# Kernel tuning notes

Hardware: AMD Instinct MI355X
Metric: run time of the kernel (lower is better)

## Reference

```python
import jax, jax.numpy as jnp
import numpy as np

NUM_PHONEMES = 512
D = 128  # embed_dim == hidden_channels == out_channels (forced by residuals)
N = 50000
E = 500000
PAD_ID = 0
LN_EPS = 1e-5


def setup_inputs() -> dict:
    key = jax.random.key(0)
    ks = jax.random.split(key, 12)
    node_ids = jax.random.randint(ks[0], (N,), 0, NUM_PHONEMES)
    edge_index = jax.random.randint(ks[1], (2, E), 0, N)
    emb = jax.random.normal(ks[2], (NUM_PHONEMES, D), jnp.float32) * 0.05
    emb = emb.at[PAD_ID].set(0.0)  # padding_idx row zeroed
    W1 = jax.random.normal(ks[3], (D, D), jnp.float32) * (1.0 / np.sqrt(D))
    b1 = jnp.zeros((D,), jnp.float32)
    W2 = jax.random.normal(ks[4], (D, D), jnp.float32) * (1.0 / np.sqrt(D))
    b2 = jnp.zeros((D,), jnp.float32)
    g1 = jnp.ones((D,), jnp.float32)
    beta1 = jnp.zeros((D,), jnp.float32)
    g2 = jnp.ones((D,), jnp.float32)
    beta2 = jnp.zeros((D,), jnp.float32)
    return {"node_ids": node_ids, "edge_index": edge_index, "emb": emb,
            "W1": W1, "b1": b1, "W2": W2, "b2": b2,
            "g1": g1, "beta1": beta1, "g2": g2, "beta2": beta2}


def _gcn_conv(x, src, dst, W, b):
    """PyG GCNConv with add_self_loops=True, normalize=True.
    out = D^{-1/2} (A + I) D^{-1/2} (x W) + b, deg computed after self-loops."""
    n = x.shape[0]
    loop = jnp.arange(n, dtype=src.dtype)
    src_f = jnp.concatenate([src, loop])  # [E+N]
    dst_f = jnp.concatenate([dst, loop])
    deg = jax.ops.segment_sum(jnp.ones_like(dst_f, dtype=x.dtype), dst_f,
                              num_segments=n)  # >=1 due to self-loops
    dis = jax.lax.rsqrt(deg)
    norm = dis[src_f] * dis[dst_f]  # [E+N]
    h = x @ W  # [N, D_out]
    msg = h[src_f] * norm[:, None]  # [E+N, D_out] gather (memory-bound)
    out = jax.ops.segment_sum(msg, dst_f, num_segments=n)  # scatter-add
    return out + b


def _layernorm(x, g, b):
    mu = jnp.mean(x, axis=-1, keepdims=True)
    var = jnp.mean(jnp.square(x - mu), axis=-1, keepdims=True)
    return (x - mu) * jax.lax.rsqrt(var + LN_EPS) * g + b


def reference(node_ids, edge_index, emb, W1, b1, W2, b2, g1, beta1, g2, beta2):
    src, dst = edge_index[0], edge_index[1]
    x = emb[node_ids]  # embedding lookup [N, D]
    h1 = _gcn_conv(x, src, dst, W1, b1)
    x = _layernorm(x + h1, g1, beta1)  # dropout is identity in eval mode
    h2 = _gcn_conv(x, src, dst, W2, b2)
    x = _layernorm(x + h2, g2, beta2)
    return x
```

## Files before the change

kernel.cpp:

```cpp
#include <hip/hip_runtime.h>

#define DD 128
#define CAP 32
#define SPILL_MAX 4096

typedef __attribute__((ext_vector_type(8))) short short8;
typedef __attribute__((ext_vector_type(4))) float float4v;

static __device__ __forceinline__ unsigned short f2bf(float x) {
    unsigned u = __builtin_bit_cast(unsigned, x);
    u += 0x7fffu + ((u >> 16) & 1u);
    return (unsigned short)(u >> 16);
}
static __device__ __forceinline__ float bflo(unsigned u) {
    return __builtin_bit_cast(float, u << 16);
}
static __device__ __forceinline__ float bfhi(unsigned u) {
    return __builtin_bit_cast(float, u & 0xffff0000u);
}

__global__ __launch_bounds__(256) void k_init(const float* __restrict__ emb,
                                              const float* __restrict__ W1,
                                              const float* __restrict__ W2,
                                              unsigned* __restrict__ embW1b,
                                              unsigned short* __restrict__ Wb,
                                              int* __restrict__ zero_dst, int NZ) {
    int blk = blockIdx.x;
    if (blk < 128) {
        int w = threadIdx.x >> 6;
        int t = threadIdx.x & 63;
        int p = blk * 4 + w;
        int c0 = t * 2, c1 = t * 2 + 1;
        float s0 = 0.f, s1 = 0.f;
#pragma unroll 8
        for (int k = 0; k < DD; k++) {
            float e = emb[p * DD + k];
            s0 += e * W1[k * DD + c0];
            s1 += e * W1[k * DD + c1];
        }
        embW1b[p * 64 + t] = (unsigned)f2bf(s0) | ((unsigned)f2bf(s1) << 16);
    } else if (blk < 136) {
        int t = (blk - 128) * 256 + threadIdx.x;
        int nt = t >> 8, ks = (t >> 6) & 3, lane = t & 63;
        int n = nt * 16 + (lane & 15);
        int kbase = ks * 32 + (lane >> 4) * 8;
        unsigned short* o = Wb + (size_t)t * 8;
#pragma unroll
        for (int j = 0; j < 8; j++)
            o[j] = f2bf(W2[(kbase + j) * DD + n]);
    } else {
        int base = (blk - 136) * 1024 + threadIdx.x * 4;
        if (base + 3 < NZ) {
            *(int4*)(zero_dst + base) = make_int4(0, 0, 0, 0);
        } else {
            if (base + 0 < NZ) zero_dst[base + 0] = 0;
            if (base + 1 < NZ) zero_dst[base + 1] = 0;
            if (base + 2 < NZ) zero_dst[base + 2] = 0;
        }
    }
}

__global__ void k_bucket(const int* __restrict__ src, const int* __restrict__ dst,
                         const int* __restrict__ node_ids,
                         int* __restrict__ cursor, unsigned* __restrict__ recs,
                         int* __restrict__ spillCnt, int* __restrict__ spill_d,
                         int* __restrict__ spill_r, int E) {
    int base = (blockIdx.x * blockDim.x + threadIdx.x) * 4;
    if (base >= E) return;
#pragma unroll
    for (int u = 0; u < 4; u++) {
        int e = base + u;
        if (e >= E) break;
        int s = src[e], d = dst[e];
        unsigned rec = (unsigned)s | ((unsigned)node_ids[s] << 16);
        int pos = atomicAdd(&cursor[d], 1);
        if (pos < CAP) {
            recs[(size_t)d * CAP + pos] = rec;
        } else {
            int sp = atomicAdd(spillCnt, 1);
            if (sp < SPILL_MAX) { spill_d[sp] = d; spill_r[sp] = (int)rec; }
        }
    }
}

__global__ __launch_bounds__(256) void k_node1g(const int* __restrict__ cursor,
                                                const unsigned* __restrict__ recs,
                                                const int* __restrict__ node_ids,
                                                const float* __restrict__ emb,
                                                const unsigned* __restrict__ embW1b,
                                                const int* __restrict__ spillCnt,
                                                const int* __restrict__ spill_d,
                                                const int* __restrict__ spill_r,
                                                const float* __restrict__ b1,
                                                const float* __restrict__ g1,
                                                const float* __restrict__ beta1,
                                                const unsigned short* __restrict__ Wb,
                                                unsigned* __restrict__ x1b,
                                                unsigned short* __restrict__ hb, int N) {
    __shared__ unsigned tile[16 * 68];
    int wv = threadIdx.x >> 6;
    int lane = threadIdx.x & 63;
    int qtr = lane >> 4;
    int l = lane & 15;
    int qbase = lane & 48;
    int base16 = blockIdx.x * 16;
    int i = base16 + wv * 4 + qtr;
    if (i < N) {
        int dg = cursor[i];
        int r0 = i * CAP;
        int r1 = r0 + ((dg < CAP) ? dg : CAP);
        int c = l * 8;
        float a0 = 0.f, a1 = 0.f, a2 = 0.f, a3 = 0.f, a4 = 0.f, a5 = 0.f, a6 = 0.f, a7 = 0.f;
        for (int j0 = r0; j0 < r1; j0 += 16) {
            int pidx = j0 + l;
            unsigned rv = recs[(pidx < r1) ? pidx : (r1 - 1)];
            int lim = r1 - j0;
#pragma unroll
            for (int q = 0; q < 16; q++) {
                unsigned rec = __shfl(rv, qbase + q, 64);
                int s = rec & 0xFFFFu;
                float n = rsqrtf((float)cursor[s] + 1.0f);
                n = (q < lim) ? n : 0.f;
                uint4 a = *(const uint4*)(embW1b + ((rec >> 16) & 511u) * 64 + l * 4);
                a0 += bflo(a.x) * n; a1 += bfhi(a.x) * n;
                a2 += bflo(a.y) * n; a3 += bfhi(a.y) * n;
                a4 += bflo(a.z) * n; a5 += bfhi(a.z) * n;
                a6 += bflo(a.w) * n; a7 += bfhi(a.w) * n;
            }
        }
        if (dg > CAP) {
            int sc = *spillCnt; if (sc > SPILL_MAX) sc = SPILL_MAX;
            for (int j = 0; j < sc; j++) {
                if (spill_d[j] == i) {
                    unsigned rec = (unsigned)spill_r[j];
                    int s = rec & 0xFFFFu;
                    float n = rsqrtf((float)cursor[s] + 1.0f);
                    uint4 a = *(const uint4*)(embW1b + ((rec >> 16) & 511u) * 64 + l * 4);
                    a0 += bflo(a.x) * n; a1 += bfhi(a.x) * n;
                    a2 += bflo(a.y) * n; a3 += bfhi(a.y) * n;
                    a4 += bflo(a.z) * n; a5 += bfhi(a.z) * n;
                    a6 += bflo(a.w) * n; a7 += bfhi(a.w) * n;
                }
            }
        }
        float di = rsqrtf((float)dg + 1.0f);
        int pid = node_ids[i];
        float4 ev0 = *(const float4*)(emb + (size_t)pid * DD + c);
        float4 ev1 = *(const float4*)(emb + (size_t)pid * DD + c + 4);
        uint4 hw = *(const uint4*)(embW1b + pid * 64 + l * 4);
        float4 bb0 = *(const float4*)(b1 + c);
        float4 bb1 = *(const float4*)(b1 + c + 4);
        float v0 = ev0.x + di * (a0 + di * bflo(hw.x)) + bb0.x;
        float v1 = ev0.y + di * (a1 + di * bfhi(hw.x)) + bb0.y;
        float v2 = ev0.z + di * (a2 + di * bflo(hw.y)) + bb0.z;
        float v3 = ev0.w + di * (a3 + di * bfhi(hw.y)) + bb0.w;
        float v4 = ev1.x + di * (a4 + di * bflo(hw.z)) + bb1.x;
        float v5 = ev1.y + di * (a5 + di * bfhi(hw.z)) + bb1.y;
        float v6 = ev1.z + di * (a6 + di * bflo(hw.w)) + bb1.z;
        float v7 = ev1.w + di * (a7 + di * bfhi(hw.w)) + bb1.w;
        float sum = v0 + v1 + v2 + v3 + v4 + v5 + v6 + v7;
#pragma unroll
        for (int o = 8; o >= 1; o >>= 1) sum += __shfl_xor(sum, o, 64);
        float mu = sum * (1.f / DD);
        float d0 = v0 - mu, d1 = v1 - mu, d2 = v2 - mu, d3 = v3 - mu;
        float d4 = v4 - mu, d5 = v5 - mu, d6 = v6 - mu, d7 = v7 - mu;
        float ss = d0 * d0 + d1 * d1 + d2 * d2 + d3 * d3 + d4 * d4 + d5 * d5 + d6 * d6 + d7 * d7;
#pragma unroll
        for (int o = 8; o >= 1; o >>= 1) ss += __shfl_xor(ss, o, 64);
        float r = rsqrtf(ss * (1.f / DD) + 1e-5f);
        float4 gg0 = *(const float4*)(g1 + c);
        float4 gg1 = *(const float4*)(g1 + c + 4);
        float4 be0 = *(const float4*)(beta1 + c);
        float4 be1 = *(const float4*)(beta1 + c + 4);
        float o0 = d0 * r * gg0.x + be0.x;
        float o1 = d1 * r * gg0.y + be0.y;
        float o2 = d2 * r * gg0.z + be0.z;
        float o3 = d3 * r * gg0.w + be0.w;
        float o4 = d4 * r * gg1.x + be1.x;
        float o5 = d5 * r * gg1.y + be1.y;
        float o6 = d6 * r * gg1.z + be1.z;
        float o7 = d7 * r * gg1.w + be1.w;
        uint4 pk;
        pk.x = (unsigned)f2bf(o0) | ((unsigned)f2bf(o1) << 16);
        pk.y = (unsigned)f2bf(o2) | ((unsigned)f2bf(o3) << 16);
        pk.z = (unsigned)f2bf(o4) | ((unsigned)f2bf(o5) << 16);
        pk.w = (unsigned)f2bf(o6) | ((unsigned)f2bf(o7) << 16);
        *(uint4*)(x1b + (size_t)i * 64 + l * 4) = pk;
        *(uint4*)(tile + (wv * 4 + qtr) * 68 + l * 4) = pk;
    }
    __syncthreads();
    int m = l;
    int quad = qtr;
    short8 afr[4];
    const char* tb = (const char*)tile;
#pragma unroll
    for (int ks = 0; ks < 4; ks++)
        afr[ks] = *(const short8*)(tb + m * 272 + ks * 64 + quad * 16);
    float dr[4];
    {
        int rb = base16 + quad * 4;
        const int4 cv = *(const int4*)(cursor + rb);
        dr[0] = rsqrtf((float)cv.x + 1.f);
        dr[1] = rsqrtf((float)cv.y + 1.f);
        dr[2] = rsqrtf((float)cv.z + 1.f);
        dr[3] = rsqrtf((float)cv.w + 1.f);
    }
    const short8* bp = (const short8*)Wb;
#pragma unroll
    for (int t = 0; t < 2; t++) {
        int nt = wv * 2 + t;
        float4v acc = {0.f, 0.f, 0.f, 0.f};
#pragma unroll
        for (int ks = 0; ks < 4; ks++) {
            short8 bfr = bp[(nt * 4 + ks) * 64 + lane];
            acc = __builtin_amdgcn_mfma_f32_16x16x32_bf16(afr[ks], bfr, acc, 0, 0, 0);
        }
        int col = nt * 16 + m;
#pragma unroll
        for (int r = 0; r < 4; r++) {
            int row = base16 + quad * 4 + r;
            if (row < N) hb[(size_t)row * DD + col] = f2bf(acc[r] * dr[r]);
        }
    }
}

__global__ __launch_bounds__(256) void k_node2(const int* __restrict__ cursor,
                                               const unsigned* __restrict__ recs,
                                               const unsigned* __restrict__ x1b,
                                               const unsigned* __restrict__ h2b,
                                               const int* __restrict__ spillCnt,
                                               const int* __restrict__ spill_d,
                                               const int* __restrict__ spill_r,
                                               const float* __restrict__ b2,
                                               const float* __restrict__ g2,
                                               const float* __restrict__ beta2,
                                               float* __restrict__ out, int N) {
    int gid = blockIdx.x * blockDim.x + threadIdx.x;
    int wave = gid >> 6;
    int lane = threadIdx.x & 63;
    int qtr = lane >> 4;
    int l = lane & 15;
    int qbase = lane & 48;
    int i = wave * 4 + qtr;
    if (i >= N) return;
    int dg = cursor[i];
    int r0 = i * CAP;
    int r1 = r0 + ((dg < CAP) ? dg : CAP);
    int c = l * 8;
    float a0 = 0.f, a1 = 0.f, a2 = 0.f, a3 = 0.f, a4 = 0.f, a5 = 0.f, a6 = 0.f, a7 = 0.f;
    for (int j0 = r0; j0 < r1; j0 += 16) {
        int pidx = j0 + l;
        unsigned rv = recs[(pidx < r1) ? pidx : (r1 - 1)];
        int lim = r1 - j0;
#pragma unroll
        for (int q = 0; q < 16; q++) {
            unsigned s = __shfl(rv, qbase + q, 64) & 0xFFFFu;
            float w = (q < lim) ? 1.f : 0.f;
            uint4 a = *(const uint4*)(h2b + (size_t)s * 64 + l * 4);
            a0 += bflo(a.x) * w; a1 += bfhi(a.x) * w;
            a2 += bflo(a.y) * w; a3 += bfhi(a.y) * w;
            a4 += bflo(a.z) * w; a5 += bfhi(a.z) * w;
            a6 += bflo(a.w) * w; a7 += bfhi(a.w) * w;
        }
    }
    if (dg > CAP) {
        int sc = *spillCnt; if (sc > SPILL_MAX) sc = SPILL_MAX;
        for (int j = 0; j < sc; j++) {
            if (spill_d[j] == i) {
                unsigned s = (unsigned)spill_r[j] & 0xFFFFu;
                uint4 a = *(const uint4*)(h2b + (size_t)s * 64 + l * 4);
                a0 += bflo(a.x); a1 += bfhi(a.x);
                a2 += bflo(a.y); a3 += bfhi(a.y);
                a4 += bflo(a.z); a5 += bfhi(a.z);
                a6 += bflo(a.w); a7 += bfhi(a.w);
            }
        }
    }
    float di = rsqrtf((float)dg + 1.0f);
    uint4 xv = *(const uint4*)(x1b + (size_t)i * 64 + l * 4);
    uint4 hv = *(const uint4*)(h2b + (size_t)i * 64 + l * 4);
    float4 bb0 = *(const float4*)(b2 + c);
    float4 bb1 = *(const float4*)(b2 + c + 4);
    float v0 = bflo(xv.x) + di * (a0 + bflo(hv.x)) + bb0.x;
    float v1 = bfhi(xv.x) + di * (a1 + bfhi(hv.x)) + bb0.y;
    float v2 = bflo(xv.y) + di * (a2 + bflo(hv.y)) + bb0.z;
    float v3 = bfhi(xv.y) + di * (a3 + bfhi(hv.y)) + bb0.w;
    float v4 = bflo(xv.z) + di * (a4 + bflo(hv.z)) + bb1.x;
    float v5 = bfhi(xv.z) + di * (a5 + bfhi(hv.z)) + bb1.y;
    float v6 = bflo(xv.w) + di * (a6 + bflo(hv.w)) + bb1.z;
    float v7 = bfhi(xv.w) + di * (a7 + bfhi(hv.w)) + bb1.w;
    float sum = v0 + v1 + v2 + v3 + v4 + v5 + v6 + v7;
#pragma unroll
    for (int o = 8; o >= 1; o >>= 1) sum += __shfl_xor(sum, o, 64);
    float mu = sum * (1.f / DD);
    float d0 = v0 - mu, d1 = v1 - mu, d2 = v2 - mu, d3 = v3 - mu;
    float d4 = v4 - mu, d5 = v5 - mu, d6 = v6 - mu, d7 = v7 - mu;
    float ss = d0 * d0 + d1 * d1 + d2 * d2 + d3 * d3 + d4 * d4 + d5 * d5 + d6 * d6 + d7 * d7;
#pragma unroll
    for (int o = 8; o >= 1; o >>= 1) ss += __shfl_xor(ss, o, 64);
    float r = rsqrtf(ss * (1.f / DD) + 1e-5f);
    float4 gg0 = *(const float4*)(g2 + c);
    float4 gg1 = *(const float4*)(g2 + c + 4);
    float4 be0 = *(const float4*)(beta2 + c);
    float4 be1 = *(const float4*)(beta2 + c + 4);
    float4 o0, o1;
    o0.x = d0 * r * gg0.x + be0.x;
    o0.y = d1 * r * gg0.y + be0.y;
    o0.z = d2 * r * gg0.z + be0.z;
    o0.w = d3 * r * gg0.w + be0.w;
    o1.x = d4 * r * gg1.x + be1.x;
    o1.y = d5 * r * gg1.y + be1.y;
    o1.z = d6 * r * gg1.z + be1.z;
    o1.w = d7 * r * gg1.w + be1.w;
    *(float4*)(out + (size_t)i * DD + c) = o0;
    *(float4*)(out + (size_t)i * DD + c + 4) = o1;
}

extern "C" void kernel_launch(void* const* d_in, const int* in_sizes, int n_in,
                              void* d_out, int out_size, void* d_ws, size_t ws_size,
                              hipStream_t stream) {
    const int* node_ids = (const int*)d_in[0];
    const int* edge_index = (const int*)d_in[1];
    const float* emb   = (const float*)d_in[2];
    const float* W1    = (const float*)d_in[3];
    const float* b1    = (const float*)d_in[4];
    const float* W2    = (const float*)d_in[5];
    const float* b2    = (const float*)d_in[6];
    const float* g2    = (const float*)d_in[9];
    const float* g1    = (const float*)d_in[7];
    const float* beta1 = (const float*)d_in[8];
    const float* beta2 = (const float*)d_in[10];
    const int N = in_sizes[0];
    const int E = in_sizes[1] / 2;
    const int* srcp = edge_index;
    const int* dstp = edge_index + E;
    float* out = (float*)d_out;

    char* base = (char*)d_ws;
    size_t off = 0;
    auto carve = [&](size_t bytes) -> void* {
        void* p = base + off;
        off += (bytes + 255) & ~(size_t)255;
        return p;
    };
    int*      meta   = (int*)carve((size_t)(N + 17) * 4);
    int*      cursor = meta;
    int*      spillCnt = meta + N + 16;
    int*      spill_d = (int*)carve((size_t)SPILL_MAX * 4);
    int*      spill_r = (int*)carve((size_t)SPILL_MAX * 4);
    unsigned* recs   = (unsigned*)carve((size_t)N * CAP * 4);
    unsigned* embW1b = (unsigned*)carve((size_t)512 * 64 * 4);
    unsigned* x1b    = (unsigned*)carve((size_t)(N + 16) * 64 * 4);
    unsigned* h2b    = (unsigned*)carve((size_t)(N + 16) * 64 * 4);
    unsigned short* Wb = (unsigned short*)carve((size_t)DD * DD * 2);
    (void)ws_size; (void)n_in; (void)out_size;

    const int TB = 256;
    const int NZ = N + 17;
    const int Zb = (NZ + 1023) / 1024;

    k_init<<<136 + Zb, TB, 0, stream>>>(emb, W1, W2, embW1b, Wb, meta, NZ);
    k_bucket<<<(E + 1023) / 1024, TB, 0, stream>>>(srcp, dstp, node_ids, cursor, recs,
                                                   spillCnt, spill_d, spill_r, E);

    int blocks16 = (N + 15) / 16;
    k_node1g<<<blocks16, TB, 0, stream>>>(cursor, recs, node_ids, emb, embW1b,
                                          spillCnt, spill_d, spill_r,
                                          b1, g1, beta1, Wb, x1b, (unsigned short*)h2b, N);
    k_node2<<<blocks16, TB, 0, stream>>>(cursor, recs, x1b, h2b,
                                         spillCnt, spill_d, spill_r,
                                         b2, g2, beta2, out, N);
}
```

Baseline: 176.3 us.

## Aggregate-then-transform in layer two and fold edge bucketing into init kernel

Layer two now sums neighbor rows of x1 first, scaled by the symmetric norm, and then applies W2 with MFMA inside the same kernel that does the residual and LayerNorm. This removes the separate transformed-feature buffer h2b and its global write and read. Layer one becomes a plain gather+LayerNorm kernel with no MFMA. Edge bucketing moves into the init kernel as extra blocks, and the cursor zeroing becomes a hipMemsetAsync. The aggregated features are rounded to bf16 before the matmul, which adds a little rounding error.

```diff
diff --git a/kernel.cpp b/kernel.cpp
--- a/kernel.cpp
+++ b/kernel.cpp
@@ -24,7 +24,14 @@
                                               const float* __restrict__ W2,
                                               unsigned* __restrict__ embW1b,
                                               unsigned short* __restrict__ Wb,
-                                              int* __restrict__ zero_dst, int NZ) {
+                                              const int* __restrict__ src,
+                                              const int* __restrict__ dst,
+                                              const int* __restrict__ node_ids,
+                                              int* __restrict__ cursor,
+                                              unsigned* __restrict__ recs,
+                                              int* __restrict__ spillCnt,
+                                              int* __restrict__ spill_d,
+                                              int* __restrict__ spill_r, int E) {
     int blk = blockIdx.x;
     if (blk < 128) {
         int w = threadIdx.x >> 6;
@@ -49,192 +56,37 @@
         for (int j = 0; j < 8; j++)
             o[j] = f2bf(W2[(kbase + j) * DD + n]);
     } else {
-        int base = (blk - 136) * 1024 + threadIdx.x * 4;
-        if (base + 3 < NZ) {
-            *(int4*)(zero_dst + base) = make_int4(0, 0, 0, 0);
-        } else {
-            if (base + 0 < NZ) zero_dst[base + 0] = 0;
-            if (base + 1 < NZ) zero_dst[base + 1] = 0;
-            if (base + 2 < NZ) zero_dst[base + 2] = 0;
-        }
-    }
-}
-
-__global__ void k_bucket(const int* __restrict__ src, const int* __restrict__ dst,
-                         const int* __restrict__ node_ids,
-                         int* __restrict__ cursor, unsigned* __restrict__ recs,
-                         int* __restrict__ spillCnt, int* __restrict__ spill_d,
-                         int* __restrict__ spill_r, int E) {
-    int base = (blockIdx.x * blockDim.x + threadIdx.x) * 4;
-    if (base >= E) return;
-#pragma unroll
-    for (int u = 0; u < 4; u++) {
-        int e = base + u;
-        if (e >= E) break;
-        int s = src[e], d = dst[e];
-        unsigned rec = (unsigned)s | ((unsigned)node_ids[s] << 16);
-        int pos = atomicAdd(&cursor[d], 1);
-        if (pos < CAP) {
-            recs[(size_t)d * CAP + pos] = rec;
-        } else {
-            int sp = atomicAdd(spillCnt, 1);
-            if (sp < SPILL_MAX) { spill_d[sp] = d; spill_r[sp] = (int)rec; }
-        }
-    }
-}
-
-__global__ __launch_bounds__(256) void k_node1g(const int* __restrict__ cursor,
-                                                const unsigned* __restrict__ recs,
-                                                const int* __restrict__ node_ids,
-                                                const float* __restrict__ emb,
-                                                const unsigned* __restrict__ embW1b,
-                                                const int* __restrict__ spillCnt,
-                                                const int* __restrict__ spill_d,
-                                                const int* __restrict__ spill_r,
-                                                const float* __restrict__ b1,
-                                                const float* __restrict__ g1,
-                                                const float* __restrict__ beta1,
-                                                const unsigned short* __restrict__ Wb,
-                                                unsigned* __restrict__ x1b,
-                                                unsigned short* __restrict__ hb, int N) {
-    __shared__ unsigned tile[16 * 68];
-    int wv = threadIdx.x >> 6;
-    int lane = threadIdx.x & 63;
-    int qtr = lane >> 4;
-    int l = lane & 15;
-    int qbase = lane & 48;
-    int base16 = blockIdx.x * 16;
-    int i = base16 + wv * 4 + qtr;
-    if (i < N) {
-        int dg = cursor[i];
-        int r0 = i * CAP;
-        int r1 = r0 + ((dg < CAP) ? dg : CAP);
-        int c = l * 8;
-        float a0 = 0.f, a1 = 0.f, a2 = 0.f, a3 = 0.f, a4 = 0.f, a5 = 0.f, a6 = 0.f, a7 = 0.f;
-        for (int j0 = r0; j0 < r1; j0 += 16) {
-            int pidx = j0 + l;
-            unsigned rv = recs[(pidx < r1) ? pidx : (r1 - 1)];
-            int lim = r1 - j0;
-#pragma unroll
-            for (int q = 0; q < 16; q++) {
-                unsigned rec = __shfl(rv, qbase + q, 64);
-                int s = rec & 0xFFFFu;
-                float n = rsqrtf((float)cursor[s] + 1.0f);
-                n = (q < lim) ? n : 0.f;
-                uint4 a = *(const uint4*)(embW1b + ((rec >> 16) & 511u) * 64 + l * 4);
-                a0 += bflo(a.x) * n; a1 += bfhi(a.x) * n;
-                a2 += bflo(a.y) * n; a3 += bfhi(a.y) * n;
-                a4 += bflo(a.z) * n; a5 += bfhi(a.z) * n;
-                a6 += bflo(a.w) * n; a7 += bfhi(a.w) * n;
-            }
-        }
-        if (dg > CAP) {
-            int sc = *spillCnt; if (sc > SPILL_MAX) sc = SPILL_MAX;
-            for (int j = 0; j < sc; j++) {
-                if (spill_d[j] == i) {
-                    unsigned rec = (unsigned)spill_r[j];
-                    int s = rec & 0xFFFFu;
-                    float n = rsqrtf((float)cursor[s] + 1.0f);
-                    uint4 a = *(const uint4*)(embW1b + ((rec >> 16) & 511u) * 64 + l * 4);
-                    a0 += bflo(a.x) * n; a1 += bfhi(a.x) * n;
-                    a2 += bflo(a.y) * n; a3 += bfhi(a.y) * n;
-                    a4 += bflo(a.z) * n; a5 += bfhi(a.z) * n;
-                    a6 += bflo(a.w) * n; a7 += bfhi(a.w) * n;
-                }
-            }
-        }
-        float di = rsqrtf((float)dg + 1.0f);
-        int pid = node_ids[i];
-        float4 ev0 = *(const float4*)(emb + (size_t)pid * DD + c);
-        float4 ev1 = *(const float4*)(emb + (size_t)pid * DD + c + 4);
-        uint4 hw = *(const uint4*)(embW1b + pid * 64 + l * 4);
-        float4 bb0 = *(const float4*)(b1 + c);
-        float4 bb1 = *(const float4*)(b1 + c + 4);
-        float v0 = ev0.x + di * (a0 + di * bflo(hw.x)) + bb0.x;
-        float v1 = ev0.y + di * (a1 + di * bfhi(hw.x)) + bb0.y;
-        float v2 = ev0.z + di * (a2 + di * bflo(hw.y)) + bb0.z;
-        float v3 = ev0.w + di * (a3 + di * bfhi(hw.y)) + bb0.w;
-        float v4 = ev1.x + di * (a4 + di * bflo(hw.z)) + bb1.x;
-        float v5 = ev1.y + di * (a5 + di * bfhi(hw.z)) + bb1.y;
-        float v6 = ev1.z + di * (a6 + di * bflo(hw.w)) + bb1.z;
-        float v7 = ev1.w + di * (a7 + di * bfhi(hw.w)) + bb1.w;
-        float sum = v0 + v1 + v2 + v3 + v4 + v5 + v6 + v7;
-#pragma unroll
-        for (int o = 8; o >= 1; o >>= 1) sum += __shfl_xor(sum, o, 64);
-        float mu = sum * (1.f / DD);
-        float d0 = v0 - mu, d1 = v1 - mu, d2 = v2 - mu, d3 = v3 - mu;
-        float d4 = v4 - mu, d5 = v5 - mu, d6 = v6 - mu, d7 = v7 - mu;
-        float ss = d0 * d0 + d1 * d1 + d2 * d2 + d3 * d3 + d4 * d4 + d5 * d5 + d6 * d6 + d7 * d7;
-#pragma unroll
-        for (int o = 8; o >= 1; o >>= 1) ss += __shfl_xor(ss, o, 64);
-        float r = rsqrtf(ss * (1.f / DD) + 1e-5f);
-        float4 gg0 = *(const float4*)(g1 + c);
-        float4 gg1 = *(const float4*)(g1 + c + 4);
-        float4 be0 = *(const float4*)(beta1 + c);
-        float4 be1 = *(const float4*)(beta1 + c + 4);
-        float o0 = d0 * r * gg0.x + be0.x;
-        float o1 = d1 * r * gg0.y + be0.y;
-        float o2 = d2 * r * gg0.z + be0.z;
-        float o3 = d3 * r * gg0.w + be0.w;
-        float o4 = d4 * r * gg1.x + be1.x;
-        float o5 = d5 * r * gg1.y + be1.y;
-        float o6 = d6 * r * gg1.z + be1.z;
-        float o7 = d7 * r * gg1.w + be1.w;
-        uint4 pk;
-        pk.x = (unsigned)f2bf(o0) | ((unsigned)f2bf(o1) << 16);
-        pk.y = (unsigned)f2bf(o2) | ((unsigned)f2bf(o3) << 16);
-        pk.z = (unsigned)f2bf(o4) | ((unsigned)f2bf(o5) << 16);
-        pk.w = (unsigned)f2bf(o6) | ((unsigned)f2bf(o7) << 16);
-        *(uint4*)(x1b + (size_t)i * 64 + l * 4) = pk;
-        *(uint4*)(tile + (wv * 4 + qtr) * 68 + l * 4) = pk;
-    }
-    __syncthreads();
-    int m = l;
-    int quad = qtr;
-    short8 afr[4];
-    const char* tb = (const char*)tile;
-#pragma unroll
-    for (int ks = 0; ks < 4; ks++)
-        afr[ks] = *(const short8*)(tb + m * 272 + ks * 64 + quad * 16);
-    float dr[4];
-    {
-        int rb = base16 + quad * 4;
-        const int4 cv = *(const int4*)(cursor + rb);
-        dr[0] = rsqrtf((float)cv.x + 1.f);
-        dr[1] = rsqrtf((float)cv.y + 1.f);
-        dr[2] = rsqrtf((float)cv.z + 1.f);
-        dr[3] = rsqrtf((float)cv.w + 1.f);
-    }
-    const short8* bp = (const short8*)Wb;
-#pragma unroll
-    for (int t = 0; t < 2; t++) {
-        int nt = wv * 2 + t;
-        float4v acc = {0.f, 0.f, 0.f, 0.f};
-#pragma unroll
-        for (int ks = 0; ks < 4; ks++) {
-            short8 bfr = bp[(nt * 4 + ks) * 64 + lane];
-            acc = __builtin_amdgcn_mfma_f32_16x16x32_bf16(afr[ks], bfr, acc, 0, 0, 0);
-        }
-        int col = nt * 16 + m;
-#pragma unroll
-        for (int r = 0; r < 4; r++) {
-            int row = base16 + quad * 4 + r;
-            if (row < N) hb[(size_t)row * DD + col] = f2bf(acc[r] * dr[r]);
-        }
-    }
-}
-
-__global__ __launch_bounds__(256) void k_node2(const int* __restrict__ cursor,
+        int base = ((blk - 136) * 256 + threadIdx.x) * 4;
+        if (base >= E) return;
+#pragma unroll
+        for (int u = 0; u < 4; u++) {
+            int e = base + u;
+            if (e >= E) break;
+            int s = src[e], d = dst[e];
+            unsigned rec = (unsigned)s | ((unsigned)node_ids[s] << 16);
+            int pos = atomicAdd(&cursor[d], 1);
+            if (pos < CAP) {
+                recs[(size_t)d * CAP + pos] = rec;
+            } else {
+                int sp = atomicAdd(spillCnt, 1);
+                if (sp < SPILL_MAX) { spill_d[sp] = d; spill_r[sp] = (int)rec; }
+            }
+        }
+    }
+}
+
+__global__ __launch_bounds__(256) void k_node1(const int* __restrict__ cursor,
                                                const unsigned* __restrict__ recs,
-                                               const unsigned* __restrict__ x1b,
-                                               const unsigned* __restrict__ h2b,
+                                               const int* __restrict__ node_ids,
+                                               const float* __restrict__ emb,
+                                               const unsigned* __restrict__ embW1b,
                                                const int* __restrict__ spillCnt,
                                                const int* __restrict__ spill_d,
                                                const int* __restrict__ spill_r,
-                                               const float* __restrict__ b2,
-                                               const float* __restrict__ g2,
-                                               const float* __restrict__ beta2,
-                                               float* __restrict__ out, int N) {
+                                               const float* __restrict__ b1,
+                                               const float* __restrict__ g1,
+                                               const float* __restrict__ beta1,
+                                               unsigned* __restrict__ x1b, int N) {
     int gid = blockIdx.x * blockDim.x + threadIdx.x;
     int wave = gid >> 6;
     int lane = threadIdx.x & 63;
@@ -254,41 +106,203 @@
         int lim = r1 - j0;
 #pragma unroll
         for (int q = 0; q < 16; q++) {
-            unsigned s = __shfl(rv, qbase + q, 64) & 0xFFFFu;
-            float w = (q < lim) ? 1.f : 0.f;
-            uint4 a = *(const uint4*)(h2b + (size_t)s * 64 + l * 4);
-            a0 += bflo(a.x) * w; a1 += bfhi(a.x) * w;
-            a2 += bflo(a.y) * w; a3 += bfhi(a.y) * w;
-            a4 += bflo(a.z) * w; a5 += bfhi(a.z) * w;
-            a6 += bflo(a.w) * w; a7 += bfhi(a.w) * w;
+            unsigned rec = __shfl(rv, qbase + q, 64);
+            int s = rec & 0xFFFFu;
+            float n = rsqrtf((float)cursor[s] + 1.0f);
+            n = (q < lim) ? n : 0.f;
+            uint4 a = *(const uint4*)(embW1b + ((rec >> 16) & 511u) * 64 + l * 4);
+            a0 += bflo(a.x) * n; a1 += bfhi(a.x) * n;
+            a2 += bflo(a.y) * n; a3 += bfhi(a.y) * n;
+            a4 += bflo(a.z) * n; a5 += bfhi(a.z) * n;
+            a6 += bflo(a.w) * n; a7 += bfhi(a.w) * n;
         }
     }
     if (dg > CAP) {
         int sc = *spillCnt; if (sc > SPILL_MAX) sc = SPILL_MAX;
         for (int j = 0; j < sc; j++) {
             if (spill_d[j] == i) {
-                unsigned s = (unsigned)spill_r[j] & 0xFFFFu;
-                uint4 a = *(const uint4*)(h2b + (size_t)s * 64 + l * 4);
-                a0 += bflo(a.x); a1 += bfhi(a.x);
-                a2 += bflo(a.y); a3 += bfhi(a.y);
-                a4 += bflo(a.z); a5 += bfhi(a.z);
-                a6 += bflo(a.w); a7 += bfhi(a.w);
+                unsigned rec = (unsigned)spill_r[j];
+                int s = rec & 0xFFFFu;
+                float n = rsqrtf((float)cursor[s] + 1.0f);
+                uint4 a = *(const uint4*)(embW1b + ((rec >> 16) & 511u) * 64 + l * 4);
+                a0 += bflo(a.x) * n; a1 += bfhi(a.x) * n;
+                a2 += bflo(a.y) * n; a3 += bfhi(a.y) * n;
+                a4 += bflo(a.z) * n; a5 += bfhi(a.z) * n;
+                a6 += bflo(a.w) * n; a7 += bfhi(a.w) * n;
             }
         }
     }
     float di = rsqrtf((float)dg + 1.0f);
-    uint4 xv = *(const uint4*)(x1b + (size_t)i * 64 + l * 4);
-    uint4 hv = *(const uint4*)(h2b + (size_t)i * 64 + l * 4);
-    float4 bb0 = *(const float4*)(b2 + c);
-    float4 bb1 = *(const float4*)(b2 + c + 4);
-    float v0 = bflo(xv.x) + di * (a0 + bflo(hv.x)) + bb0.x;
-    float v1 = bfhi(xv.x) + di * (a1 + bfhi(hv.x)) + bb0.y;
-    float v2 = bflo(xv.y) + di * (a2 + bflo(hv.y)) + bb0.z;
-    float v3 = bfhi(xv.y) + di * (a3 + bfhi(hv.y)) + bb0.w;
-    float v4 = bflo(xv.z) + di * (a4 + bflo(hv.z)) + bb1.x;
-    float v5 = bfhi(xv.z) + di * (a5 + bfhi(hv.z)) + bb1.y;
-    float v6 = bflo(xv.w) + di * (a6 + bflo(hv.w)) + bb1.z;
-    float v7 = bfhi(xv.w) + di * (a7 + bfhi(hv.w)) + bb1.w;
+    int pid = node_ids[i];
+    float4 ev0 = *(const float4*)(emb + (size_t)pid * DD + c);
+    float4 ev1 = *(const float4*)(emb + (size_t)pid * DD + c + 4);
+    uint4 hw = *(const uint4*)(embW1b + pid * 64 + l * 4);
+    float4 bb0 = *(const float4*)(b1 + c);
+    float4 bb1 = *(const float4*)(b1 + c + 4);
+    float v0 = ev0.x + di * (a0 + di * bflo(hw.x)) + bb0.x;
+    float v1 = ev0.y + di * (a1 + di * bfhi(hw.x)) + bb0.y;
+    float v2 = ev0.z + di * (a2 + di * bflo(hw.y)) + bb0.z;
+    float v3 = ev0.w + di * (a3 + di * bfhi(hw.y)) + bb0.w;
+    float v4 = ev1.x + di * (a4 + di * bflo(hw.z)) + bb1.x;
+    float v5 = ev1.y + di * (a5 + di * bfhi(hw.z)) + bb1.y;
+    float v6 = ev1.z + di * (a6 + di * bflo(hw.w)) + bb1.z;
+    float v7 = ev1.w + di * (a7 + di * bfhi(hw.w)) + bb1.w;
+    float sum = v0 + v1 + v2 + v3 + v4 + v5 + v6 + v7;
+#pragma unroll
+    for (int o = 8; o >= 1; o >>= 1) sum += __shfl_xor(sum, o, 64);
+    float mu = sum * (1.f / DD);
+    float d0 = v0 - mu, d1 = v1 - mu, d2 = v2 - mu, d3 = v3 - mu;
+    float d4 = v4 - mu, d5 = v5 - mu, d6 = v6 - mu, d7 = v7 - mu;
+    float ss = d0 * d0 + d1 * d1 + d2 * d2 + d3 * d3 + d4 * d4 + d5 * d5 + d6 * d6 + d7 * d7;
+#pragma unroll
+    for (int o = 8; o >= 1; o >>= 1) ss += __shfl_xor(ss, o, 64);
+    float r = rsqrtf(ss * (1.f / DD) + 1e-5f);
+    float4 gg0 = *(const float4*)(g1 + c);
+    float4 gg1 = *(const float4*)(g1 + c + 4);
+    float4 be0 = *(const float4*)(beta1 + c);
+    float4 be1 = *(const float4*)(beta1 + c + 4);
+    float o0 = d0 * r * gg0.x + be0.x;
+    float o1 = d1 * r * gg0.y + be0.y;
+    float o2 = d2 * r * gg0.z + be0.z;
+    float o3 = d3 * r * gg0.w + be0.w;
+    float o4 = d4 * r * gg1.x + be1.x;
+    float o5 = d5 * r * gg1.y + be1.y;
+    float o6 = d6 * r * gg1.z + be1.z;
+    float o7 = d7 * r * gg1.w + be1.w;
+    uint4 pk;
+    pk.x = (unsigned)f2bf(o0) | ((unsigned)f2bf(o1) << 16);
+    pk.y = (unsigned)f2bf(o2) | ((unsigned)f2bf(o3) << 16);
+    pk.z = (unsigned)f2bf(o4) | ((unsigned)f2bf(o5) << 16);
+    pk.w = (unsigned)f2bf(o6) | ((unsigned)f2bf(o7) << 16);
+    *(uint4*)(x1b + (size_t)i * 64 + l * 4) = pk;
+}
+
+__global__ __launch_bounds__(256) void k_node2(const int* __restrict__ cursor,
+                                               const unsigned* __restrict__ recs,
+                                               const unsigned* __restrict__ x1b,
+                                               const int* __restrict__ spillCnt,
+                                               const int* __restrict__ spill_d,
+                                               const int* __restrict__ spill_r,
+                                               const float* __restrict__ b2,
+                                               const float* __restrict__ g2,
+                                               const float* __restrict__ beta2,
+                                               const unsigned short* __restrict__ Wb,
+                                               float* __restrict__ out, int N) {
+    __shared__ unsigned tileA[16 * 68];
+    __shared__ float tileH[16 * 132];
+    int wv = threadIdx.x >> 6;
+    int lane = threadIdx.x & 63;
+    int qtr = lane >> 4;
+    int l = lane & 15;
+    int qbase = lane & 48;
+    int base16 = blockIdx.x * 16;
+    int i = base16 + wv * 4 + qtr;
+    uint4 xv = make_uint4(0, 0, 0, 0);
+    float bb[8] = {0, 0, 0, 0, 0, 0, 0, 0};
+    int c = l * 8;
+    if (i < N) {
+        int dg = cursor[i];
+        int r0 = i * CAP;
+        int r1 = r0 + ((dg < CAP) ? dg : CAP);
+        float a0 = 0.f, a1 = 0.f, a2 = 0.f, a3 = 0.f, a4 = 0.f, a5 = 0.f, a6 = 0.f, a7 = 0.f;
+        for (int j0 = r0; j0 < r1; j0 += 16) {
+            int pidx = j0 + l;
+            unsigned rv = recs[(pidx < r1) ? pidx : (r1 - 1)];
+            int lim = r1 - j0;
+#pragma unroll
+            for (int q = 0; q < 16; q++) {
+                unsigned s = __shfl(rv, qbase + q, 64) & 0xFFFFu;
+                float n = rsqrtf((float)cursor[s] + 1.0f);
+                n = (q < lim) ? n : 0.f;
+                uint4 a = *(const uint4*)(x1b + (size_t)s * 64 + l * 4);
+                a0 += bflo(a.x) * n; a1 += bfhi(a.x) * n;
+                a2 += bflo(a.y) * n; a3 += bfhi(a.y) * n;
+                a4 += bflo(a.z) * n; a5 += bfhi(a.z) * n;
+                a6 += bflo(a.w) * n; a7 += bfhi(a.w) * n;
+            }
+        }
+        if (dg > CAP) {
+            int sc = *spillCnt; if (sc > SPILL_MAX) sc = SPILL_MAX;
+            for (int j = 0; j < sc; j++) {
+                if (spill_d[j] == i) {
+                    unsigned s = (unsigned)spill_r[j] & 0xFFFFu;
+                    float n = rsqrtf((float)cursor[s] + 1.0f);
+                    uint4 a = *(const uint4*)(x1b + (size_t)s * 64 + l * 4);
+                    a0 += bflo(a.x) * n; a1 += bfhi(a.x) * n;
+                    a2 += bflo(a.y) * n; a3 += bfhi(a.y) * n;
+                    a4 += bflo(a.z) * n; a5 += bfhi(a.z) * n;
+                    a6 += bflo(a.w) * n; a7 += bfhi(a.w) * n;
+                }
+            }
+        }
+        float di = rsqrtf((float)dg + 1.0f);
+        xv = *(const uint4*)(x1b + (size_t)i * 64 + l * 4);
+        float z0 = a0 + di * bflo(xv.x);
+        float z1 = a1 + di * bfhi(xv.x);
+        float z2 = a2 + di * bflo(xv.y);
+        float z3 = a3 + di * bfhi(xv.y);
+        float z4 = a4 + di * bflo(xv.z);
+        float z5 = a5 + di * bfhi(xv.z);
+        float z6 = a6 + di * bflo(xv.w);
+        float z7 = a7 + di * bfhi(xv.w);
+        uint4 pk;
+        pk.x = (unsigned)f2bf(z0) | ((unsigned)f2bf(z1) << 16);
+        pk.y = (unsigned)f2bf(z2) | ((unsigned)f2bf(z3) << 16);
+        pk.z = (unsigned)f2bf(z4) | ((unsigned)f2bf(z5) << 16);
+        pk.w = (unsigned)f2bf(z6) | ((unsigned)f2bf(z7) << 16);
+        *(uint4*)(tileA + (wv * 4 + qtr) * 68 + l * 4) = pk;
+        float4 t0 = *(const float4*)(b2 + c);
+        float4 t1 = *(const float4*)(b2 + c + 4);
+        bb[0] = t0.x; bb[1] = t0.y; bb[2] = t0.z; bb[3] = t0.w;
+        bb[4] = t1.x; bb[5] = t1.y; bb[6] = t1.z; bb[7] = t1.w;
+    }
+    __syncthreads();
+    {
+        int m = l;
+        int quad = qtr;
+        short8 afr[4];
+        const char* tb = (const char*)tileA;
+#pragma unroll
+        for (int ks = 0; ks < 4; ks++)
+            afr[ks] = *(const short8*)(tb + m * 272 + ks * 64 + quad * 16);
+        float dr[4];
+        {
+            int rb = base16 + quad * 4;
+            const int4 cv = *(const int4*)(cursor + rb);
+            dr[0] = rsqrtf((float)cv.x + 1.f);
+            dr[1] = rsqrtf((float)cv.y + 1.f);
+            dr[2] = rsqrtf((float)cv.z + 1.f);
+            dr[3] = rsqrtf((float)cv.w + 1.f);
+        }
+        const short8* bp = (const short8*)Wb;
+#pragma unroll
+        for (int t = 0; t < 2; t++) {
+            int nt = wv * 2 + t;
+            float4v acc = {0.f, 0.f, 0.f, 0.f};
+#pragma unroll
+            for (int ks = 0; ks < 4; ks++) {
+                short8 bfr = bp[(nt * 4 + ks) * 64 + lane];
+                acc = __builtin_amdgcn_mfma_f32_16x16x32_bf16(afr[ks], bfr, acc, 0, 0, 0);
+            }
+            int col = nt * 16 + m;
+#pragma unroll
+            for (int r = 0; r < 4; r++)
+                tileH[(quad * 4 + r) * 132 + col] = acc[r] * dr[r];
+        }
+    }
+    __syncthreads();
+    if (i >= N) return;
+    int row_local = wv * 4 + qtr;
+    float4 h0 = *(const float4*)(tileH + row_local * 132 + c);
+    float4 h1 = *(const float4*)(tileH + row_local * 132 + c + 4);
+    float v0 = bflo(xv.x) + h0.x + bb[0];
+    float v1 = bfhi(xv.x) + h0.y + bb[1];
+    float v2 = bflo(xv.y) + h0.z + bb[2];
+    float v3 = bfhi(xv.y) + h0.w + bb[3];
+    float v4 = bflo(xv.z) + h1.x + bb[4];
+    float v5 = bfhi(xv.z) + h1.y + bb[5];
+    float v6 = bflo(xv.w) + h1.z + bb[6];
+    float v7 = bfhi(xv.w) + h1.w + bb[7];
     float sum = v0 + v1 + v2 + v3 + v4 + v5 + v6 + v7;
 #pragma unroll
     for (int o = 8; o >= 1; o >>= 1) sum += __shfl_xor(sum, o, 64);
@@ -326,9 +340,9 @@
     const float* b1    = (const float*)d_in[4];
     const float* W2    = (const float*)d_in[5];
     const float* b2    = (const float*)d_in[6];
-    const float* g2    = (const float*)d_in[9];
     const float* g1    = (const float*)d_in[7];
     const float* beta1 = (const float*)d_in[8];
+    const float* g2    = (const float*)d_in[9];
     const float* beta2 = (const float*)d_in[10];
     const int N = in_sizes[0];
     const int E = in_sizes[1] / 2;
@@ -351,23 +365,24 @@
     unsigned* recs   = (unsigned*)carve((size_t)N * CAP * 4);
     unsigned* embW1b = (unsigned*)carve((size_t)512 * 64 * 4);
     unsigned* x1b    = (unsigned*)carve((size_t)(N + 16) * 64 * 4);
-    unsigned* h2b    = (unsigned*)carve((size_t)(N + 16) * 64 * 4);
     unsigned short* Wb = (unsigned short*)carve((size_t)DD * DD * 2);
     (void)ws_size; (void)n_in; (void)out_size;
 
     const int TB = 256;
-    const int NZ = N + 17;
-    const int Zb = (NZ + 1023) / 1024;
-
-    k_init<<<136 + Zb, TB, 0, stream>>>(emb, W1, W2, embW1b, Wb, meta, NZ);
-    k_bucket<<<(E + 1023) / 1024, TB, 0, stream>>>(srcp, dstp, node_ids, cursor, recs,
-                                                   spillCnt, spill_d, spill_r, E);
-
+    const int Hb = (E + 1023) / 1024;
+
+    hipMemsetAsync(meta, 0, (size_t)(N + 17) * 4, stream);
+    k_init<<<136 + Hb, TB, 0, stream>>>(emb, W1, W2, embW1b, Wb,
+                                        srcp, dstp, node_ids, cursor, recs,
+                                        spillCnt, spill_d, spill_r, E);
+
+    long long tn = (long long)((N + 3) / 4) * 64;
+    int nodeBlocks = (int)((tn + TB - 1) / TB);
+    k_node1<<<nodeBlocks, TB, 0, stream>>>(cursor, recs, node_ids, emb, embW1b,
+                                           spillCnt, spill_d, spill_r,
+                                           b1, g1, beta1, x1b, N);
     int blocks16 = (N + 15) / 16;
-    k_node1g<<<blocks16, TB, 0, stream>>>(cursor, recs, node_ids, emb, embW1b,
-                                          spillCnt, spill_d, spill_r,
-                                          b1, g1, beta1, Wb, x1b, (unsigned short*)h2b, N);
-    k_node2<<<blocks16, TB, 0, stream>>>(cursor, recs, x1b, h2b,
+    k_node2<<<blocks16, TB, 0, stream>>>(cursor, recs, x1b,
                                          spillCnt, spill_d, spill_r,
-                                         b2, g2, beta2, out, N);
-}
+                                         b2, g2, beta2, Wb, out, N);
+}
```

New measurement: 192.9 us. 1.09x slower.
